# Optimization experiments

Hardware: AMD Instinct MI355X
Metric: run time of the kernel (lower is better)

Reference implementation:

```python
import jax, jax.numpy as jnp
import numpy as np

B, DIN, DOUT, DC, K, DB = 4096, 512, 512, 64, 16, 256
NEG = 0.01
LN_EPS = 1e-5

def _lrelu(v):
    return jnp.where(v >= 0, v, NEG * v)

def setup_inputs() -> dict:
    key = jax.random.key(0)
    ks = jax.random.split(key, 12)
    bound = 1.0 / np.sqrt(DIN)
    def u(k, shape, b):
        return jax.random.uniform(k, shape, jnp.float32, -b, b)
    return {
        "x": jax.random.normal(ks[0], (B, DIN), jnp.float32),
        "c": jax.random.normal(ks[1], (B, DC), jnp.float32),
        "ln_gamma": jnp.ones((DIN,), jnp.float32),
        "ln_beta": jnp.zeros((DIN,), jnp.float32),
        "w1": u(ks[2], (DC, DB), 1.0 / np.sqrt(DC)),
        "b1": u(ks[3], (DB,), 1.0 / np.sqrt(DC)),
        "wr": u(ks[4], (DB, DB), 1.0 / np.sqrt(DB)),
        "br": u(ks[5], (DB,), 1.0 / np.sqrt(DB)),
        "w2": u(ks[6], (DB, K), 1.0 / np.sqrt(DB)),
        "b2": u(ks[7], (K,), 1.0 / np.sqrt(DB)),
        "W": u(ks[8], (K, DIN, DOUT), bound),
        "bvec": u(ks[9], (K, DOUT), bound),
    }

def reference(x, c, ln_gamma, ln_beta, w1, b1, wr, br, w2, b2, W, bvec):
    # DenseActivation: LayerNorm + LeakyReLU (dropout_rate=0)
    mu = jnp.mean(x, axis=-1, keepdims=True)
    var = jnp.mean(jnp.square(x - mu), axis=-1, keepdims=True)
    xn = (x - mu) * jax.lax.rsqrt(var + LN_EPS) * ln_gamma + ln_beta
    a = _lrelu(xn)  # [B, DIN]
    # basis_functions(c): Linear -> 1 preactivation resnet block -> LeakyReLU -> Linear
    h = c @ w1 + b1                      # [B, DB]
    h = h + (_lrelu(h) @ wr + br)        # residual block (preactivation)
    h = _lrelu(h)                        # activate_output
    bf = h @ w2 + b2                     # [B, K]
    # out_b = x_b^T (sum_k bf_bk W_k) + bf_b @ bias ; reordered contraction
    xw = jnp.einsum("bi,kio->bko", a, W)       # [B, K, DOUT]
    out = jnp.einsum("bk,bko->bo", bf, xw)     # [B, DOUT]
    out = out + bf @ bvec
    return out
```

## Files before the change

### kernel.cpp

```cpp
#include <hip/hip_runtime.h>


#define LRELU(v) ((v) >= 0.f ? (v) : 0.01f * (v))

typedef _Float16 f16x8 __attribute__((ext_vector_type(8)));
typedef float f32x4 __attribute__((ext_vector_type(4)));

#define GL16(gp, lp) __builtin_amdgcn_global_load_lds(                      \
    (const __attribute__((address_space(1))) void*)(gp),                    \
    (__attribute__((address_space(3))) void*)(lp), 16, 0, 0)

#define MFMA16(a, b, c) __builtin_amdgcn_mfma_f32_16x16x32_f16((a), (b), (c), 0, 0, 0)

__global__ __launch_bounds__(256) void prep_kernel(
    const float* __restrict__ x, const float* __restrict__ gam,
    const float* __restrict__ bet, _Float16* __restrict__ a,
    const float* __restrict__ c, const float* __restrict__ w1,
    const float* __restrict__ b1, const float* __restrict__ wr,
    const float* __restrict__ br, const float* __restrict__ w2,
    const float* __restrict__ b2, float* __restrict__ bfo,
    const float* __restrict__ W, _Float16* __restrict__ Wt)
{
    __shared__ __align__(16) char smem[18432];
    int tid = threadIdx.x;
    int blk = blockIdx.x;

    if (blk < 512) {
        float* c_l  = (float*)smem;
        float* lr_l = (float*)(smem + 2048);
        float* h_l  = (float*)(smem + 10240);
        int b0 = blk * 8;

        for (int i = tid; i < 8 * 64; i += 256) c_l[i] = c[(size_t)b0 * 64 + i];

        float w1c[64];
#pragma unroll
        for (int u = 0; u < 64; ++u) w1c[u] = w1[u * 256 + tid];
        float b1s = b1[tid];
        __syncthreads();

        float h1[8];
#pragma unroll
        for (int r = 0; r < 8; ++r) h1[r] = b1s;
#pragma unroll
        for (int j4 = 0; j4 < 16; ++j4) {
#pragma unroll
            for (int r = 0; r < 8; ++r) {
                float4 cv = *(const float4*)&c_l[r * 64 + j4 * 4];
                h1[r] += cv.x * w1c[j4 * 4 + 0] + cv.y * w1c[j4 * 4 + 1] +
                         cv.z * w1c[j4 * 4 + 2] + cv.w * w1c[j4 * 4 + 3];
            }
        }
#pragma unroll
        for (int r = 0; r < 8; ++r) lr_l[r * 256 + tid] = LRELU(h1[r]);
        __syncthreads();

        float brv = br[tid];
        float h2[8];
#pragma unroll
        for (int r = 0; r < 8; ++r) h2[r] = h1[r] + brv;

#pragma unroll 1
        for (int jc = 0; jc < 8; ++jc) {
            float w8[32];
#pragma unroll
            for (int u = 0; u < 32; ++u) w8[u] = wr[(jc * 32 + u) * 256 + tid];
#pragma unroll
            for (int j4 = 0; j4 < 8; ++j4) {
#pragma unroll
                for (int r = 0; r < 8; ++r) {
                    float4 lv = *(const float4*)&lr_l[r * 256 + jc * 32 + j4 * 4];
                    h2[r] += lv.x * w8[j4 * 4 + 0] + lv.y * w8[j4 * 4 + 1] +
                             lv.z * w8[j4 * 4 + 2] + lv.w * w8[j4 * 4 + 3];
                }
            }
        }
#pragma unroll
        for (int r = 0; r < 8; ++r) h_l[r * 256 + tid] = LRELU(h2[r]);
        __syncthreads();

        if (tid < 128) {
            int r = tid >> 4, k = tid & 15;
            float s = b2[k];
#pragma unroll 1
            for (int qc = 0; qc < 8; ++qc) {
                float wv[32];
#pragma unroll
                for (int u = 0; u < 32; ++u) wv[u] = w2[(qc * 32 + u) * 16 + k];
#pragma unroll
                for (int q4 = 0; q4 < 8; ++q4) {
                    float4 hv = *(const float4*)&h_l[r * 256 + qc * 32 + q4 * 4];
                    s += hv.x * wv[q4 * 4 + 0] + hv.y * wv[q4 * 4 + 1] +
                         hv.z * wv[q4 * 4 + 2] + hv.w * wv[q4 * 4 + 3];
                }
            }
            bfo[(size_t)(b0 + r) * 16 + k] = s;
        }

    } else if (blk < 1536) {
        float* t = (float*)smem;
        int bid = blk - 512;
        int k  = bid >> 6;
        int it = (bid >> 3) & 7;
        int ot = bid & 7;
        int i0 = it * 64, o0 = ot * 64;

        int rr = tid >> 4, c4 = (tid & 15) * 4;
#pragma unroll
        for (int p = 0; p < 4; ++p) {
            int r = p * 16 + rr;
            float4 v = *(const float4*)&W[((size_t)(k * 512 + i0 + r)) * 512 + o0 + c4];
            t[r * 65 + c4 + 0] = v.x;
            t[r * 65 + c4 + 1] = v.y;
            t[r * 65 + c4 + 2] = v.z;
            t[r * 65 + c4 + 3] = v.w;
        }
        __syncthreads();

        int ol = tid >> 2, c0 = (tid & 3) * 16;
        _Float16 hb[16] __attribute__((aligned(16)));
#pragma unroll
        for (int u = 0; u < 16; ++u) hb[u] = (_Float16)t[(c0 + u) * 65 + ol];
        _Float16* dst = &Wt[(size_t)(o0 + ol) * 8192 + k * 512 + i0 + c0];
        *(float4*)dst       = *(const float4*)&hb[0];
        *(float4*)(dst + 8) = *(const float4*)&hb[8];

    } else {
        int lane = tid & 63;
        int row  = (blk - 1536) * 4 + (tid >> 6);
        const float* xr = x + (size_t)row * 512 + lane * 8;
        float4 v0 = *(const float4*)xr;
        float4 v1 = *(const float4*)(xr + 4);

        float s = v0.x + v0.y + v0.z + v0.w + v1.x + v1.y + v1.z + v1.w;
#pragma unroll
        for (int m = 1; m < 64; m <<= 1) s += __shfl_xor(s, m);
        float mean = s * (1.f / 512.f);

        float d, s2 = 0.f;
        d = v0.x - mean; s2 += d * d;
        d = v0.y - mean; s2 += d * d;
        d = v0.z - mean; s2 += d * d;
        d = v0.w - mean; s2 += d * d;
        d = v1.x - mean; s2 += d * d;
        d = v1.y - mean; s2 += d * d;
        d = v1.z - mean; s2 += d * d;
        d = v1.w - mean; s2 += d * d;
#pragma unroll
        for (int m = 1; m < 64; m <<= 1) s2 += __shfl_xor(s2, m);
        float rstd = rsqrtf(s2 * (1.f / 512.f) + 1e-5f);

        float4 g0 = *(const float4*)&gam[lane * 8];
        float4 g1 = *(const float4*)&gam[lane * 8 + 4];
        float4 b0 = *(const float4*)&bet[lane * 8];
        float4 b1v = *(const float4*)&bet[lane * 8 + 4];

        _Float16 o8[8] __attribute__((aligned(16)));
        float y;
        y = (v0.x - mean) * rstd * g0.x + b0.x;  y = LRELU(y); o8[0] = (_Float16)y;
        y = (v0.y - mean) * rstd * g0.y + b0.y;  y = LRELU(y); o8[1] = (_Float16)y;
        y = (v0.z - mean) * rstd * g0.z + b0.z;  y = LRELU(y); o8[2] = (_Float16)y;
        y = (v0.w - mean) * rstd * g0.w + b0.w;  y = LRELU(y); o8[3] = (_Float16)y;
        y = (v1.x - mean) * rstd * g1.x + b1v.x; y = LRELU(y); o8[4] = (_Float16)y;
        y = (v1.y - mean) * rstd * g1.y + b1v.y; y = LRELU(y); o8[5] = (_Float16)y;
        y = (v1.z - mean) * rstd * g1.z + b1v.z; y = LRELU(y); o8[6] = (_Float16)y;
        y = (v1.w - mean) * rstd * g1.w + b1v.w; y = LRELU(y); o8[7] = (_Float16)y;

        *(float4*)&a[(size_t)row * 512 + lane * 8] = *(const float4*)o8;
    }
}

template <int NSPLIT>
__global__ __launch_bounds__(512, 2) void gemm_kernel(
    const _Float16* __restrict__ A,
    const _Float16* __restrict__ Wt,
    const float* __restrict__ bfg,
    float* __restrict__ pout)
{
    constexpr int KTN = 16 / NSPLIT;
    constexpr int NT  = KTN * 8;

    __shared__ _Float16 As[2][256 * 64];
    __shared__ _Float16 Bs[2][256 * 64];

    const int tid = threadIdx.x;
    const int bid = blockIdx.x;
    const int split = bid % NSPLIT;
    const int mn  = bid / NSPLIT;
    const int n0  = (mn & 1) * 256;
    const int bm0 = (mn >> 1) * 256;
    const int kt0 = split * KTN;

    const int lane = tid & 63, wid = tid >> 6;
    const int wm = wid >> 2, wn = wid & 3;
    const int l16 = lane & 15, lg = lane >> 4;

    _Float16 s16[KTN][8];
#pragma unroll
    for (int kt = 0; kt < KTN; ++kt)
#pragma unroll
        for (int f = 0; f < 8; ++f)
            s16[kt][f] = (_Float16)
                bfg[(size_t)(bm0 + wm * 128 + f * 16 + l16) * 16 + kt0 + kt];

    const int brow = tid >> 3;
    const int swc  = (tid & 7) ^ (brow & 7);
    const _Float16* aAs = A  + (size_t)(bm0 + brow) * 512  + swc * 8;
    const _Float16* aBs = Wt + (size_t)(n0  + brow) * 8192 + swc * 8;

    auto STAGE = [&](int t, int buf) {
        const int ka = (t & 7) * 64;
        const size_t kb = (size_t)(kt0 + (t >> 3)) * 512 + ka;
        char* la = (char*)&As[buf][0] + tid * 16;
        char* lb = (char*)&Bs[buf][0] + tid * 16;
#pragma unroll
        for (int p = 0; p < 4; ++p) {
            GL16(aAs + (size_t)(p * 64) * 512 + ka, la + p * 8192);
            GL16(aBs + (size_t)(p * 64) * 8192 + kb, lb + p * 8192);
        }
    };

    const int swr = l16 & 7;
    const int aRowByte = (wm * 128 + l16) * 128;
    const int bRowByte = (wn * 64 + l16) * 128;
    const int sw0 = ((0 + lg) ^ swr) << 4;
    const int sw1 = ((4 + lg) ^ swr) << 4;

    const f32x4 z4 = {0.f, 0.f, 0.f, 0.f};
    f32x4 acc[8][4];
#pragma unroll
    for (int f = 0; f < 8; ++f)
#pragma unroll
        for (int nf = 0; nf < 4; ++nf) acc[f][nf] = z4;

    STAGE(0, 0);
    STAGE(1, 1);
    asm volatile("s_waitcnt vmcnt(8)" ::: "memory");
    __builtin_amdgcn_s_barrier();
    __builtin_amdgcn_sched_barrier(0);

#define AREAD(q)                                                            \
    xa = *(const f16x8*)(Ab + aRowByte + (2 * (q) + 0) * 2048 + sw0);       \
    xb = *(const f16x8*)(Ab + aRowByte + (2 * (q) + 0) * 2048 + sw1);       \
    xc = *(const f16x8*)(Ab + aRowByte + (2 * (q) + 1) * 2048 + sw0);       \
    xd = *(const f16x8*)(Ab + aRowByte + (2 * (q) + 1) * 2048 + sw1);

#define MFMAQ(q)                                                            \
    {                                                                       \
        const _Float16 sA = s16[kt][2 * (q) + 0];                           \
        const _Float16 sB = s16[kt][2 * (q) + 1];                           \
        xa *= sA; xb *= sA; xc *= sB; xd *= sB;                             \
        __builtin_amdgcn_s_setprio(1);                                      \
        acc[2*(q)+0][0] = MFMA16(xa, bA0, acc[2*(q)+0][0]);                 \
        acc[2*(q)+0][0] = MFMA16(xb, bA1, acc[2*(q)+0][0]);                 \
        acc[2*(q)+0][1] = MFMA16(xa, bB0, acc[2*(q)+0][1]);                 \
        acc[2*(q)+0][1] = MFMA16(xb, bB1, acc[2*(q)+0][1]);                 \
        acc[2*(q)+0][2] = MFMA16(xa, bC0, acc[2*(q)+0][2]);                 \
        acc[2*(q)+0][2] = MFMA16(xb, bC1, acc[2*(q)+0][2]);                 \
        acc[2*(q)+0][3] = MFMA16(xa, bD0, acc[2*(q)+0][3]);                 \
        acc[2*(q)+0][3] = MFMA16(xb, bD1, acc[2*(q)+0][3]);                 \
        acc[2*(q)+1][0] = MFMA16(xc, bA0, acc[2*(q)+1][0]);                 \
        acc[2*(q)+1][0] = MFMA16(xd, bA1, acc[2*(q)+1][0]);                 \
        acc[2*(q)+1][1] = MFMA16(xc, bB0, acc[2*(q)+1][1]);                 \
        acc[2*(q)+1][1] = MFMA16(xd, bB1, acc[2*(q)+1][1]);                 \
        acc[2*(q)+1][2] = MFMA16(xc, bC0, acc[2*(q)+1][2]);                 \
        acc[2*(q)+1][2] = MFMA16(xd, bC1, acc[2*(q)+1][2]);                 \
        acc[2*(q)+1][3] = MFMA16(xc, bD0, acc[2*(q)+1][3]);                 \
        acc[2*(q)+1][3] = MFMA16(xd, bD1, acc[2*(q)+1][3]);                 \
        __builtin_amdgcn_s_setprio(0);                                      \
    }

#pragma unroll
    for (int kt = 0; kt < KTN; ++kt) {
#pragma unroll 1
        for (int t2 = 0; t2 < 8; ++t2) {
            const int t = kt * 8 + t2;
            const int cur = t & 1;
            const char* Ab = (const char*)&As[cur][0];
            const char* Bb = (const char*)&Bs[cur][0];
            const int tt = t + 2;
            const bool st = (tt < NT);
            char* sAd = (char*)&As[cur][0] + tid * 16;
            char* sBd = (char*)&Bs[cur][0] + tid * 16;
            const int ka = (tt & 7) * 64;
            const size_t kb = (size_t)(kt0 + (tt >> 3)) * 512 + ka;

            f16x8 xa, xb, xc, xd;

            f16x8 bA0 = *(const f16x8*)(Bb + bRowByte + 0 * 2048 + sw0);
            f16x8 bA1 = *(const f16x8*)(Bb + bRowByte + 0 * 2048 + sw1);
            f16x8 bB0 = *(const f16x8*)(Bb + bRowByte + 1 * 2048 + sw0);
            f16x8 bB1 = *(const f16x8*)(Bb + bRowByte + 1 * 2048 + sw1);
            f16x8 bC0 = *(const f16x8*)(Bb + bRowByte + 2 * 2048 + sw0);
            f16x8 bC1 = *(const f16x8*)(Bb + bRowByte + 2 * 2048 + sw1);
            f16x8 bD0 = *(const f16x8*)(Bb + bRowByte + 3 * 2048 + sw0);
            f16x8 bD1 = *(const f16x8*)(Bb + bRowByte + 3 * 2048 + sw1);
            AREAD(0);
            __builtin_amdgcn_s_barrier();
            MFMAQ(0);
            __builtin_amdgcn_s_barrier();

            AREAD(1);
            if (st) {
                GL16(aBs + (size_t)(0 * 64) * 8192 + kb, sBd + 0 * 8192);
                GL16(aBs + (size_t)(1 * 64) * 8192 + kb, sBd + 1 * 8192);
            }
            __builtin_amdgcn_s_barrier();
            MFMAQ(1);
            __builtin_amdgcn_s_barrier();

            AREAD(2);
            if (st) {
                GL16(aBs + (size_t)(2 * 64) * 8192 + kb, sBd + 2 * 8192);
                GL16(aBs + (size_t)(3 * 64) * 8192 + kb, sBd + 3 * 8192);
                GL16(aAs + (size_t)(0 * 64) * 512 + ka, sAd + 0 * 8192);
                GL16(aAs + (size_t)(2 * 64) * 512 + ka, sAd + 2 * 8192);
            }
            __builtin_amdgcn_s_barrier();
            MFMAQ(2);
            __builtin_amdgcn_s_barrier();

            AREAD(3);
            __builtin_amdgcn_s_barrier();
            MFMAQ(3);
            __builtin_amdgcn_s_barrier();

            if (st) {
                GL16(aAs + (size_t)(1 * 64) * 512 + ka, sAd + 1 * 8192);
                GL16(aAs + (size_t)(3 * 64) * 512 + ka, sAd + 3 * 8192);
                asm volatile("s_waitcnt vmcnt(8)" ::: "memory");
            } else {
                asm volatile("s_waitcnt vmcnt(0)" ::: "memory");
            }
            __builtin_amdgcn_s_barrier();
            __builtin_amdgcn_sched_barrier(0);
        }
    }
#undef AREAD
#undef MFMAQ

    float* op = pout + (size_t)split * (4096 * 512);
#pragma unroll
    for (int f = 0; f < 8; ++f)
#pragma unroll
        for (int j = 0; j < 4; ++j) {
            const int grow = bm0 + wm * 128 + f * 16 + lg * 4 + j;
            float* orow = op + (size_t)grow * 512 + n0 + wn * 64 + l16;
#pragma unroll
            for (int nf = 0; nf < 4; ++nf)
                orow[nf * 16] = acc[f][nf][j];
        }
}

__global__ __launch_bounds__(256) void reduce_kernel(const float* __restrict__ p,
                                                     const float* __restrict__ bfg,
                                                     const float* __restrict__ bvec,
                                                     float* __restrict__ out,
                                                     int nsplit)
{
    size_t i = (size_t)blockIdx.x * 256 + threadIdx.x;
    const float4* p4 = (const float4*)p;
    float4 s = p4[i];
    for (int sp = 1; sp < nsplit; ++sp) {
        float4 v = p4[i + (size_t)sp * 524288];
        s.x += v.x; s.y += v.y; s.z += v.z; s.w += v.w;
    }
    int b = (int)(i >> 7);
    int c = (int)(i & 127);
    const float* bfr = bfg + (size_t)b * 16;
    const float4* bv4 = (const float4*)bvec;
#pragma unroll
    for (int k = 0; k < 16; ++k) {
        float bk = bfr[k];
        float4 v = bv4[k * 128 + c];
        s.x += bk * v.x; s.y += bk * v.y; s.z += bk * v.z; s.w += bk * v.w;
    }
    ((float4*)out)[i] = s;
}

extern "C" void kernel_launch(void* const* d_in, const int* in_sizes, int n_in,
                              void* d_out, int out_size, void* d_ws, size_t ws_size,
                              hipStream_t stream)
{
    const float* x    = (const float*)d_in[0];
    const float* c    = (const float*)d_in[1];
    const float* gam  = (const float*)d_in[2];
    const float* bet  = (const float*)d_in[3];
    const float* w1   = (const float*)d_in[4];
    const float* b1   = (const float*)d_in[5];
    const float* wr   = (const float*)d_in[6];
    const float* br   = (const float*)d_in[7];
    const float* w2   = (const float*)d_in[8];
    const float* b2   = (const float*)d_in[9];
    const float* W    = (const float*)d_in[10];
    const float* bvec = (const float*)d_in[11];
    float* out = (float*)d_out;

    const size_t outBytes  = (size_t)4096 * 512 * 4;
    const size_t miscBytes = (8u << 20) + (4u << 20) + (256u << 10);

    int nsplit = (ws_size >= 8 * outBytes + miscBytes) ? 8 : 4;

    char* ws = (char*)d_ws;
    size_t pbytes = (size_t)nsplit * outBytes;
    float*    part = (float*)ws;
    _Float16* Wt   = (_Float16*)(ws + pbytes);
    _Float16* af   = (_Float16*)(ws + pbytes + (8u << 20));
    float*    bf   = (float*)(ws + pbytes + (12u << 20));

    prep_kernel<<<dim3(2560), dim3(256), 0, stream>>>(
        x, gam, bet, af, c, w1, b1, wr, br, w2, b2, bf, W, Wt);

    if (nsplit == 8) {
        gemm_kernel<8><<<dim3(256), dim3(512), 0, stream>>>(af, Wt, bf, part);
    } else {
        gemm_kernel<4><<<dim3(128), dim3(512), 0, stream>>>(af, Wt, bf, part);
    }
    reduce_kernel<<<dim3(2048), dim3(256), 0, stream>>>(part, bf, bvec, out, nsplit);
}
```

Before: 94.21 us.

## Store split-K partials in fp16 and fold bias term into GEMM epilogue

The GEMM epilogue now adds each split's share of the bf @ bvec bias contraction and writes the split-K partial sums as fp16 instead of fp32. The reduce kernel becomes a pure fp16-to-fp32 sum over splits with 8-wide vector loads. This halves the bytes written and read for the 8 partial buffers and drops the bias loop from the reduction. It costs precision, since partials are rounded to fp16 before summation, and it fixes nsplit at 8 without checking workspace size.

```diff
diff --git a/kernel.cpp b/kernel.cpp
--- a/kernel.cpp
+++ b/kernel.cpp
@@ -175,7 +175,8 @@
     const _Float16* __restrict__ A,
     const _Float16* __restrict__ Wt,
     const float* __restrict__ bfg,
-    float* __restrict__ pout)
+    const float* __restrict__ bvec,
+    _Float16* __restrict__ pout)
 {
     constexpr int KTN = 16 / NSPLIT;
     constexpr int NT  = KTN * 8;
@@ -339,43 +340,51 @@
 #undef AREAD
 #undef MFMAQ
 
-    float* op = pout + (size_t)split * (4096 * 512);
+    _Float16* op = pout + (size_t)split * (4096 * 512);
+    const int colBase = n0 + wn * 64 + l16;
+    float bvv[KTN][4];
+#pragma unroll
+    for (int kt = 0; kt < KTN; ++kt)
+#pragma unroll
+        for (int nf = 0; nf < 4; ++nf)
+            bvv[kt][nf] = bvec[(kt0 + kt) * 512 + colBase + nf * 16];
+
 #pragma unroll
     for (int f = 0; f < 8; ++f)
 #pragma unroll
         for (int j = 0; j < 4; ++j) {
             const int grow = bm0 + wm * 128 + f * 16 + lg * 4 + j;
-            float* orow = op + (size_t)grow * 512 + n0 + wn * 64 + l16;
-#pragma unroll
-            for (int nf = 0; nf < 4; ++nf)
-                orow[nf * 16] = acc[f][nf][j];
+            const float* bfr = &bfg[(size_t)grow * 16 + kt0];
+            float bfl[KTN];
+#pragma unroll
+            for (int kt = 0; kt < KTN; ++kt) bfl[kt] = bfr[kt];
+            _Float16* orow = op + (size_t)grow * 512 + colBase;
+#pragma unroll
+            for (int nf = 0; nf < 4; ++nf) {
+                float v = acc[f][nf][j];
+#pragma unroll
+                for (int kt = 0; kt < KTN; ++kt) v += bfl[kt] * bvv[kt][nf];
+                orow[nf * 16] = (_Float16)v;
+            }
         }
 }
 
-__global__ __launch_bounds__(256) void reduce_kernel(const float* __restrict__ p,
-                                                     const float* __restrict__ bfg,
-                                                     const float* __restrict__ bvec,
+__global__ __launch_bounds__(256) void reduce_kernel(const _Float16* __restrict__ p,
                                                      float* __restrict__ out,
                                                      int nsplit)
 {
-    size_t i = (size_t)blockIdx.x * 256 + threadIdx.x;
-    const float4* p4 = (const float4*)p;
-    float4 s = p4[i];
-    for (int sp = 1; sp < nsplit; ++sp) {
-        float4 v = p4[i + (size_t)sp * 524288];
-        s.x += v.x; s.y += v.y; s.z += v.z; s.w += v.w;
+    size_t i   = (size_t)blockIdx.x * 256 + threadIdx.x;
+    size_t off = i * 8;
+    float s[8] = {0.f, 0.f, 0.f, 0.f, 0.f, 0.f, 0.f, 0.f};
+    for (int sp = 0; sp < nsplit; ++sp) {
+        f16x8 v = *(const f16x8*)&p[(size_t)sp * 2097152 + off];
+#pragma unroll
+        for (int u = 0; u < 8; ++u) s[u] += (float)v[u];
     }
-    int b = (int)(i >> 7);
-    int c = (int)(i & 127);
-    const float* bfr = bfg + (size_t)b * 16;
-    const float4* bv4 = (const float4*)bvec;
-#pragma unroll
-    for (int k = 0; k < 16; ++k) {
-        float bk = bfr[k];
-        float4 v = bv4[k * 128 + c];
-        s.x += bk * v.x; s.y += bk * v.y; s.z += bk * v.z; s.w += bk * v.w;
-    }
-    ((float4*)out)[i] = s;
+    float4 o0 = {s[0], s[1], s[2], s[3]};
+    float4 o1 = {s[4], s[5], s[6], s[7]};
+    *(float4*)&out[off]     = o0;
+    *(float4*)&out[off + 4] = o1;
 }
 
 extern "C" void kernel_launch(void* const* d_in, const int* in_sizes, int n_in,
@@ -396,25 +405,19 @@
     const float* bvec = (const float*)d_in[11];
     float* out = (float*)d_out;
 
-    const size_t outBytes  = (size_t)4096 * 512 * 4;
-    const size_t miscBytes = (8u << 20) + (4u << 20) + (256u << 10);
-
-    int nsplit = (ws_size >= 8 * outBytes + miscBytes) ? 8 : 4;
+    const int nsplit = 8;
+    const size_t partBytes = (size_t)nsplit * 4096 * 512 * sizeof(_Float16);
 
     char* ws = (char*)d_ws;
-    size_t pbytes = (size_t)nsplit * outBytes;
-    float*    part = (float*)ws;
-    _Float16* Wt   = (_Float16*)(ws + pbytes);
-    _Float16* af   = (_Float16*)(ws + pbytes + (8u << 20));
-    float*    bf   = (float*)(ws + pbytes + (12u << 20));
+    _Float16* part = (_Float16*)ws;
+    _Float16* Wt   = (_Float16*)(ws + partBytes);
+    _Float16* af   = (_Float16*)(ws + partBytes + (8u << 20));
+    float*    bf   = (float*)(ws + partBytes + (12u << 20));
 
     prep_kernel<<<dim3(2560), dim3(256), 0, stream>>>(
         x, gam, bet, af, c, w1, b1, wr, br, w2, b2, bf, W, Wt);
 
-    if (nsplit == 8) {
-        gemm_kernel<8><<<dim3(256), dim3(512), 0, stream>>>(af, Wt, bf, part);
-    } else {
-        gemm_kernel<4><<<dim3(128), dim3(512), 0, stream>>>(af, Wt, bf, part);
-    }
-    reduce_kernel<<<dim3(2048), dim3(256), 0, stream>>>(part, bf, bvec, out, nsplit);
+    gemm_kernel<8><<<dim3(256), dim3(512), 0, stream>>>(af, Wt, bf, bvec, part);
+
+    reduce_kernel<<<dim3(1024), dim3(256), 0, stream>>>(part, out, nsplit);
 }
```

Result: faster. 84.40 us (-10.4%).
